# Performance work log

Hardware: AMD Instinct MI355X
Metric: run time of the kernel (lower is better)

The kernel has to match this reference:

```python
import jax, jax.numpy as jnp
import numpy as np

N_NODES = 100000


def _gcn_norm(edge_index, num_nodes):
    # Add self-loops, then symmetric normalization D^-1/2 A D^-1/2 (PyG gcn_norm).
    loops = jnp.arange(num_nodes, dtype=edge_index.dtype)
    src = jnp.concatenate([edge_index[0], loops])
    dst = jnp.concatenate([edge_index[1], loops])
    ew = jnp.ones(src.shape[0], dtype=jnp.float32)
    deg = jax.ops.segment_sum(ew, dst, num_segments=num_nodes)
    dinv = jnp.where(deg > 0, jax.lax.rsqrt(deg), 0.0)
    norm = dinv[src] * ew * dinv[dst]
    return src, dst, norm


def _prop_gcn_conv(x, W, b, src, dst, norm, num_nodes, prop_nums):
    # PropGCNConv: linear transform once, then prop_nums hops of normalized
    # sparse propagation (gather from src, scale, scatter-add to dst), + bias.
    x = x @ W
    for _ in range(prop_nums):
        msgs = x[src] * norm[:, None]              # [E, d]
        x = jax.ops.segment_sum(msgs, dst, num_segments=num_nodes)
    return x + b


def setup_inputs() -> dict:
    key = jax.random.key(0)
    k1, k2, k3, k4 = jax.random.split(key, 4)
    in_dim, hid_dim, num_classes = 128, 64, 40
    n_edges = 800000
    x = jax.random.normal(k1, (N_NODES, in_dim), dtype=jnp.float32)
    W0 = jax.random.normal(k2, (in_dim, hid_dim), dtype=jnp.float32) * (1.0 / np.sqrt(in_dim))
    b0 = jnp.zeros((hid_dim,), dtype=jnp.float32)
    Wc = jax.random.normal(k3, (hid_dim, num_classes), dtype=jnp.float32) * (1.0 / np.sqrt(hid_dim))
    bc = jnp.zeros((num_classes,), dtype=jnp.float32)
    edge_index = jax.random.randint(k4, (2, n_edges), 0, N_NODES, dtype=jnp.int64)
    return {"x": x, "W0": W0, "b0": b0, "Wc": Wc, "bc": bc,
            "edge_index": edge_index, "prop_nums": 30}


def reference(x, W0, b0, Wc, bc, edge_index, prop_nums):
    n = x.shape[0]
    src, dst, norm = _gcn_norm(edge_index, n)
    # feat_bottleneck: conv -> relu -> dropout (eval mode -> identity)
    h = _prop_gcn_conv(x, W0, b0, src, dst, norm, n, prop_nums)
    h = jax.nn.relu(h)
    # feat_classifier: single-hop PropGCNConv
    out = _prop_gcn_conv(h, Wc, bc, src, dst, norm, n, 1)
    return out
```

## Files before the change

### kernel.cpp

```cpp
#include <hip/hip_runtime.h>

#define NN  100000
#define NE  800000
#define NNZ 900000
#define IN_DIM 128
#define HID 64
#define NC  40
#define HOPS 30

typedef _Float16 half8 __attribute__((ext_vector_type(8)));


__global__ void init_cnt_k(int* __restrict__ cnt) {
    int i = blockIdx.x * blockDim.x + threadIdx.x;
    if (i < NN) cnt[i] = 1;
}

__global__ void count_edges_k(const int* __restrict__ dst, int* __restrict__ cnt) {
    int e = blockIdx.x * blockDim.x + threadIdx.x;
    if (e < NE) atomicAdd(&cnt[dst[e]], 1);
}

__global__ void dinv_k(const int* __restrict__ cnt, float* __restrict__ dinv) {
    int i = blockIdx.x * blockDim.x + threadIdx.x;
    if (i < NN) dinv[i] = rsqrtf((float)cnt[i]);
}

__global__ void scan_blocks_k(const int* __restrict__ cnt, int* __restrict__ rp,
                              int* __restrict__ partials) {
    __shared__ int s[256];
    int tid = threadIdx.x;
    int i = blockIdx.x * 256 + tid;
    int v = (i < NN) ? cnt[i] : 0;
    s[tid] = v;
    __syncthreads();
    for (int off = 1; off < 256; off <<= 1) {
        int t = (tid >= off) ? s[tid - off] : 0;
        __syncthreads();
        s[tid] += t;
        __syncthreads();
    }
    if (i < NN) rp[i] = s[tid] - v;
    if (tid == 255) partials[blockIdx.x] = s[255];
}

__global__ void scan_partials_k(int* __restrict__ partials, int nblk) {
    if (blockIdx.x == 0 && threadIdx.x == 0) {
        int acc = 0;
        for (int b = 0; b < nblk; ++b) { int t = partials[b]; partials[b] = acc; acc += t; }
    }
}

__global__ void add_offsets_k(int* __restrict__ rp, const int* __restrict__ partials) {
    int i = blockIdx.x * 256 + threadIdx.x;
    if (i < NN) rp[i] += partials[blockIdx.x];
    if (i == 0) rp[NN] = NNZ;
}

__global__ void fill_csr_k(const int* __restrict__ src, const int* __restrict__ dst,
                           const float* __restrict__ dinv, const int* __restrict__ rp,
                           int* __restrict__ cursor, int2* __restrict__ cv) {
    int e = blockIdx.x * blockDim.x + threadIdx.x;
    if (e >= NNZ) return;
    int s, d;
    if (e < NE) { s = src[e]; d = dst[e]; }
    else        { s = d = e - NE; }
    int pos = rp[d] + atomicAdd(&cursor[d], 1);
    int2 p;
    p.x = s;
    p.y = __float_as_int(dinv[s] * dinv[d]);
    cv[pos] = p;
}


__global__ void __launch_bounds__(256, 4) gemm1_k(const float* __restrict__ x,
                                                  const float* __restrict__ W,
                                                  _Float16* __restrict__ out) {
    __shared__ float Ws[IN_DIM * HID];
    int t = threadIdx.x;
    for (int i = t; i < IN_DIM * HID / 4; i += 256)
        ((float4*)Ws)[i] = ((const float4*)W)[i];
    __syncthreads();
    int node = blockIdx.x * 256 + t;
    if (node >= NN) return;
    const float4* xr = (const float4*)(x + (size_t)node * IN_DIM);
    float4 acc[16];
#pragma unroll
    for (int c = 0; c < 16; ++c) acc[c] = make_float4(0.f, 0.f, 0.f, 0.f);
#pragma unroll 4
    for (int k4 = 0; k4 < IN_DIM / 4; ++k4) {
        float4 xv = xr[k4];
#pragma unroll
        for (int kk = 0; kk < 4; ++kk) {
            float xs = (kk == 0) ? xv.x : (kk == 1) ? xv.y : (kk == 2) ? xv.z : xv.w;
            const float4* wr = (const float4*)(Ws + (k4 * 4 + kk) * HID);
#pragma unroll
            for (int c4 = 0; c4 < 16; ++c4) {
                float4 wv = wr[c4];
                acc[c4].x = fmaf(xs, wv.x, acc[c4].x);
                acc[c4].y = fmaf(xs, wv.y, acc[c4].y);
                acc[c4].z = fmaf(xs, wv.z, acc[c4].z);
                acc[c4].w = fmaf(xs, wv.w, acc[c4].w);
            }
        }
    }
    half8* o8 = (half8*)(out + (size_t)node * HID);
#pragma unroll
    for (int g = 0; g < 8; ++g) {
        half8 o;
        float4 lo = acc[g * 2], hi = acc[g * 2 + 1];
        o[0] = (_Float16)lo.x; o[1] = (_Float16)lo.y; o[2] = (_Float16)lo.z; o[3] = (_Float16)lo.w;
        o[4] = (_Float16)hi.x; o[5] = (_Float16)hi.y; o[6] = (_Float16)hi.z; o[7] = (_Float16)hi.w;
        o8[g] = o;
    }
}

__global__ void prop64_k(const _Float16* __restrict__ xin, _Float16* __restrict__ xout,
                         const int* __restrict__ rp, const int2* __restrict__ cv) {
    int wid  = threadIdx.x >> 6;
    int lane = threadIdx.x & 63;
    int n    = lane >> 5;
    int s    = (lane >> 3) & 3;
    int f    = lane & 7;
    int node = blockIdx.x * 8 + wid * 2 + n;
    int beg = rp[node], end = rp[node + 1];
    const half8* x8 = (const half8*)xin;
    float a0 = 0.f, a1 = 0.f, a2 = 0.f, a3 = 0.f, a4 = 0.f, a5 = 0.f, a6 = 0.f, a7 = 0.f;
    for (int e = beg + s; e < end; e += 16) {
        int  e1 = e + 4,  e2 = e + 8,  e3 = e + 12;
        bool p1 = e1 < end, p2 = e2 < end, p3 = e3 < end;
        int2 q0 = cv[e];
        int2 q1 = cv[p1 ? e1 : beg];
        int2 q2 = cv[p2 ? e2 : beg];
        int2 q3 = cv[p3 ? e3 : beg];
        float v0 = __int_as_float(q0.y);
        float v1 = p1 ? __int_as_float(q1.y) : 0.f;
        float v2 = p2 ? __int_as_float(q2.y) : 0.f;
        float v3 = p3 ? __int_as_float(q3.y) : 0.f;
        half8 x0 = x8[(size_t)q0.x * 8 + f];
        half8 x1 = x8[(size_t)q1.x * 8 + f];
        half8 x2 = x8[(size_t)q2.x * 8 + f];
        half8 x3 = x8[(size_t)q3.x * 8 + f];
        a0 += v0 * (float)x0[0] + v1 * (float)x1[0] + v2 * (float)x2[0] + v3 * (float)x3[0];
        a1 += v0 * (float)x0[1] + v1 * (float)x1[1] + v2 * (float)x2[1] + v3 * (float)x3[1];
        a2 += v0 * (float)x0[2] + v1 * (float)x1[2] + v2 * (float)x2[2] + v3 * (float)x3[2];
        a3 += v0 * (float)x0[3] + v1 * (float)x1[3] + v2 * (float)x2[3] + v3 * (float)x3[3];
        a4 += v0 * (float)x0[4] + v1 * (float)x1[4] + v2 * (float)x2[4] + v3 * (float)x3[4];
        a5 += v0 * (float)x0[5] + v1 * (float)x1[5] + v2 * (float)x2[5] + v3 * (float)x3[5];
        a6 += v0 * (float)x0[6] + v1 * (float)x1[6] + v2 * (float)x2[6] + v3 * (float)x3[6];
        a7 += v0 * (float)x0[7] + v1 * (float)x1[7] + v2 * (float)x2[7] + v3 * (float)x3[7];
    }
#pragma unroll
    for (int m = 8; m <= 16; m <<= 1) {
        a0 += __shfl_xor(a0, m); a1 += __shfl_xor(a1, m);
        a2 += __shfl_xor(a2, m); a3 += __shfl_xor(a3, m);
        a4 += __shfl_xor(a4, m); a5 += __shfl_xor(a5, m);
        a6 += __shfl_xor(a6, m); a7 += __shfl_xor(a7, m);
    }
    if (s == 0) {
        half8 r;
        r[0] = (_Float16)a0; r[1] = (_Float16)a1; r[2] = (_Float16)a2; r[3] = (_Float16)a3;
        r[4] = (_Float16)a4; r[5] = (_Float16)a5; r[6] = (_Float16)a6; r[7] = (_Float16)a7;
        ((half8*)xout)[(size_t)node * 8 + f] = r;
    }
}

__global__ void __launch_bounds__(256, 4) gemm2_k(const _Float16* __restrict__ h,
                                                  const float* __restrict__ b0,
                                                  const float* __restrict__ Wc,
                                                  float* __restrict__ g) {
    __shared__ float Wcs[HID * NC];
    __shared__ float b0s[HID];
    int t = threadIdx.x;
    for (int i = t; i < HID * NC / 4; i += 256)
        ((float4*)Wcs)[i] = ((const float4*)Wc)[i];
    if (t < HID) b0s[t] = b0[t];
    __syncthreads();
    int node = blockIdx.x * 256 + t;
    if (node >= NN) return;
    const half8* hr = (const half8*)(h + (size_t)node * HID);
    float acc[NC];
#pragma unroll
    for (int c = 0; c < NC; ++c) acc[c] = 0.f;
#pragma unroll
    for (int j = 0; j < 8; ++j) {
        half8 hv = hr[j];
#pragma unroll
        for (int m = 0; m < 8; ++m) {
            int k = j * 8 + m;
            float fv = fmaxf((float)hv[m] + b0s[k], 0.f);
            const float4* wr = (const float4*)(Wcs + k * NC);
#pragma unroll
            for (int c4 = 0; c4 < NC / 4; ++c4) {
                float4 wv = wr[c4];
                acc[c4 * 4 + 0] = fmaf(fv, wv.x, acc[c4 * 4 + 0]);
                acc[c4 * 4 + 1] = fmaf(fv, wv.y, acc[c4 * 4 + 1]);
                acc[c4 * 4 + 2] = fmaf(fv, wv.z, acc[c4 * 4 + 2]);
                acc[c4 * 4 + 3] = fmaf(fv, wv.w, acc[c4 * 4 + 3]);
            }
        }
    }
    float4* go = (float4*)(g + (size_t)node * NC);
#pragma unroll
    for (int c4 = 0; c4 < NC / 4; ++c4) {
        float4 o; o.x = acc[c4 * 4 + 0]; o.y = acc[c4 * 4 + 1];
        o.z = acc[c4 * 4 + 2]; o.w = acc[c4 * 4 + 3];
        go[c4] = o;
    }
}

__global__ void prop40_k(const float* __restrict__ g, float* __restrict__ out,
                         const int* __restrict__ rp, const int2* __restrict__ cv,
                         const float* __restrict__ bc) {
    int t = blockIdx.x * 256 + threadIdx.x;
    int node = t >> 6;
    int lane = threadIdx.x & 63;
    int s = lane >> 3;
    int f = lane & 7;
    int beg = rp[node], end = rp[node + 1];
    float a0 = 0.f, a1 = 0.f, a2 = 0.f, a3 = 0.f, a4 = 0.f;
    for (int e = beg + s; e < end; e += 16) {
        int  e1 = e + 8;
        bool p1 = e1 < end;
        int2 q0 = cv[e];
        int2 q1 = cv[p1 ? e1 : beg];
        float v0 = __int_as_float(q0.y);
        float v1 = p1 ? __int_as_float(q1.y) : 0.f;
        const float* g0 = g + (size_t)q0.x * NC + f;
        const float* g1 = g + (size_t)q1.x * NC + f;
        a0 += v0 * g0[0]  + v1 * g1[0];
        a1 += v0 * g0[8]  + v1 * g1[8];
        a2 += v0 * g0[16] + v1 * g1[16];
        a3 += v0 * g0[24] + v1 * g1[24];
        a4 += v0 * g0[32] + v1 * g1[32];
    }
    for (int m = 8; m <= 32; m <<= 1) {
        a0 += __shfl_xor(a0, m); a1 += __shfl_xor(a1, m); a2 += __shfl_xor(a2, m);
        a3 += __shfl_xor(a3, m); a4 += __shfl_xor(a4, m);
    }
    if (s == 0) {
        float* o = out + (size_t)node * NC + f;
        o[0]  = a0 + bc[f];
        o[8]  = a1 + bc[f + 8];
        o[16] = a2 + bc[f + 16];
        o[24] = a3 + bc[f + 24];
        o[32] = a4 + bc[f + 32];
    }
}


extern "C" void kernel_launch(void* const* d_in, const int* in_sizes, int n_in,
                              void* d_out, int out_size, void* d_ws, size_t ws_size,
                              hipStream_t stream) {
    const float* x  = (const float*)d_in[0];
    const float* W0 = (const float*)d_in[1];
    const float* b0 = (const float*)d_in[2];
    const float* Wc = (const float*)d_in[3];
    const float* bc = (const float*)d_in[4];
    const int*   ei = (const int*)d_in[5];
    const int* src = ei;
    const int* dst = ei + NE;

    char* ws = (char*)d_ws;
    size_t off = 0;
    auto alloc = [&](size_t bytes) -> void* {
        void* p = ws + off;
        off = (off + bytes + 255) & ~(size_t)255;
        return p;
    };
    float* dinv     = (float*)alloc((size_t)NN * 4);
    int*   rp       = (int*)  alloc((size_t)(NN + 1) * 4);
    int*   cnt      = (int*)  alloc((size_t)NN * 4);
    int*   cursor   = (int*)  alloc((size_t)NN * 4);
    int*   partials = (int*)  alloc(512 * 4);
    int2*  cvp      = (int2*) alloc((size_t)NNZ * 8);
    _Float16* XA    = (_Float16*)alloc((size_t)NN * HID * 2);
    _Float16* XB    = (_Float16*)alloc((size_t)NN * HID * 2);
    float* G        = (float*)alloc((size_t)NN * NC * 4);

    const int nblk_n = (NN + 255) / 256;

    init_cnt_k   <<<nblk_n, 256, 0, stream>>>(cnt);
    count_edges_k<<<(NE + 255) / 256, 256, 0, stream>>>(dst, cnt);
    dinv_k       <<<nblk_n, 256, 0, stream>>>(cnt, dinv);
    scan_blocks_k<<<nblk_n, 256, 0, stream>>>(cnt, rp, partials);
    scan_partials_k<<<1, 64, 0, stream>>>(partials, nblk_n);
    add_offsets_k<<<nblk_n, 256, 0, stream>>>(rp, partials);
    hipMemsetAsync(cursor, 0, (size_t)NN * 4, stream);
    fill_csr_k   <<<(NNZ + 255) / 256, 256, 0, stream>>>(src, dst, dinv, rp, cursor, cvp);

    gemm1_k<<<nblk_n, 256, 0, stream>>>(x, W0, XA);

    _Float16* a = XA;
    _Float16* b = XB;
    for (int hop = 0; hop < HOPS; ++hop) {
        prop64_k<<<NN / 8, 256, 0, stream>>>(a, b, rp, cvp);
        _Float16* tmp = a; a = b; b = tmp;
    }

    gemm2_k<<<nblk_n, 256, 0, stream>>>(a, b0, Wc, G);
    prop40_k<<<NN * HID / 256, 256, 0, stream>>>(G, (float*)d_out, rp, cvp, bc);
}
```

Measured before the change: 887.6 us.

## Reuse degree counters as CSR cursors, retile gemm1, store classifier logits in fp16

The CSR build now zeroes the degree counters with a memset and folds the self-loop into later reads. It then decrements those counters to place edges, which removes the separate cursor array and the init kernel. gemm1 is retiled so each thread computes half the output columns for two nodes, sharing shared-memory weight reads across them. The classifier intermediate G is stored as fp16 and gathered as half8 vectors in the final propagation, halving that gather traffic at some precision cost.

```diff
diff --git a/kernel.cpp b/kernel.cpp
--- a/kernel.cpp
+++ b/kernel.cpp
@@ -11,11 +11,6 @@
 typedef _Float16 half8 __attribute__((ext_vector_type(8)));
 
 
-__global__ void init_cnt_k(int* __restrict__ cnt) {
-    int i = blockIdx.x * blockDim.x + threadIdx.x;
-    if (i < NN) cnt[i] = 1;
-}
-
 __global__ void count_edges_k(const int* __restrict__ dst, int* __restrict__ cnt) {
     int e = blockIdx.x * blockDim.x + threadIdx.x;
     if (e < NE) atomicAdd(&cnt[dst[e]], 1);
@@ -23,7 +18,7 @@
 
 __global__ void dinv_k(const int* __restrict__ cnt, float* __restrict__ dinv) {
     int i = blockIdx.x * blockDim.x + threadIdx.x;
-    if (i < NN) dinv[i] = rsqrtf((float)cnt[i]);
+    if (i < NN) dinv[i] = rsqrtf((float)(cnt[i] + 1));
 }
 
 __global__ void scan_blocks_k(const int* __restrict__ cnt, int* __restrict__ rp,
@@ -31,7 +26,7 @@
     __shared__ int s[256];
     int tid = threadIdx.x;
     int i = blockIdx.x * 256 + tid;
-    int v = (i < NN) ? cnt[i] : 0;
+    int v = (i < NN) ? (cnt[i] + 1) : 0;
     s[tid] = v;
     __syncthreads();
     for (int off = 1; off < 256; off <<= 1) {
@@ -59,21 +54,28 @@
 
 __global__ void fill_csr_k(const int* __restrict__ src, const int* __restrict__ dst,
                            const float* __restrict__ dinv, const int* __restrict__ rp,
-                           int* __restrict__ cursor, int2* __restrict__ cv) {
+                           int* __restrict__ cnt, int2* __restrict__ cv) {
     int e = blockIdx.x * blockDim.x + threadIdx.x;
     if (e >= NNZ) return;
-    int s, d;
-    if (e < NE) { s = src[e]; d = dst[e]; }
-    else        { s = d = e - NE; }
-    int pos = rp[d] + atomicAdd(&cursor[d], 1);
+    int pos;
     int2 p;
-    p.x = s;
-    p.y = __float_as_int(dinv[s] * dinv[d]);
+    if (e < NE) {
+        int s = src[e], d = dst[e];
+        int old = atomicAdd(&cnt[d], -1);
+        pos = rp[d] + old - 1;
+        p.x = s;
+        p.y = __float_as_int(dinv[s] * dinv[d]);
+    } else {
+        int i = e - NE;
+        pos = rp[i + 1] - 1;
+        p.x = i;
+        p.y = __float_as_int(dinv[i] * dinv[i]);
+    }
     cv[pos] = p;
 }
 
 
-__global__ void __launch_bounds__(256, 4) gemm1_k(const float* __restrict__ x,
+__global__ void __launch_bounds__(256, 2) gemm1_k(const float* __restrict__ x,
                                                   const float* __restrict__ W,
                                                   _Float16* __restrict__ out) {
     __shared__ float Ws[IN_DIM * HID];
@@ -81,37 +83,64 @@
     for (int i = t; i < IN_DIM * HID / 4; i += 256)
         ((float4*)Ws)[i] = ((const float4*)W)[i];
     __syncthreads();
-    int node = blockIdx.x * 256 + t;
-    if (node >= NN) return;
-    const float4* xr = (const float4*)(x + (size_t)node * IN_DIM);
-    float4 acc[16];
-#pragma unroll
-    for (int c = 0; c < 16; ++c) acc[c] = make_float4(0.f, 0.f, 0.f, 0.f);
-#pragma unroll 4
+    int w = t >> 6, l = t & 63;
+    int ch = w >> 1;
+    int n0 = blockIdx.x * 256 + (w & 1) * 64 + l;
+    int n1 = n0 + 128;
+    int n0c = n0 < NN ? n0 : NN - 1;
+    int n1c = n1 < NN ? n1 : NN - 1;
+    const float4* xr0 = (const float4*)(x + (size_t)n0c * IN_DIM);
+    const float4* xr1 = (const float4*)(x + (size_t)n1c * IN_DIM);
+    float4 a0[8], a1[8];
+#pragma unroll
+    for (int c = 0; c < 8; ++c) {
+        a0[c] = make_float4(0.f, 0.f, 0.f, 0.f);
+        a1[c] = make_float4(0.f, 0.f, 0.f, 0.f);
+    }
+#pragma unroll 2
     for (int k4 = 0; k4 < IN_DIM / 4; ++k4) {
-        float4 xv = xr[k4];
+        float4 xv0 = xr0[k4];
+        float4 xv1 = xr1[k4];
 #pragma unroll
         for (int kk = 0; kk < 4; ++kk) {
-            float xs = (kk == 0) ? xv.x : (kk == 1) ? xv.y : (kk == 2) ? xv.z : xv.w;
-            const float4* wr = (const float4*)(Ws + (k4 * 4 + kk) * HID);
-#pragma unroll
-            for (int c4 = 0; c4 < 16; ++c4) {
-                float4 wv = wr[c4];
-                acc[c4].x = fmaf(xs, wv.x, acc[c4].x);
-                acc[c4].y = fmaf(xs, wv.y, acc[c4].y);
-                acc[c4].z = fmaf(xs, wv.z, acc[c4].z);
-                acc[c4].w = fmaf(xs, wv.w, acc[c4].w);
+            float xs0 = (kk == 0) ? xv0.x : (kk == 1) ? xv0.y : (kk == 2) ? xv0.z : xv0.w;
+            float xs1 = (kk == 0) ? xv1.x : (kk == 1) ? xv1.y : (kk == 2) ? xv1.z : xv1.w;
+            const float4* wr = (const float4*)(Ws + (k4 * 4 + kk) * HID + ch * 32);
+#pragma unroll
+            for (int c = 0; c < 8; ++c) {
+                float4 wv = wr[c];
+                a0[c].x = fmaf(xs0, wv.x, a0[c].x);
+                a0[c].y = fmaf(xs0, wv.y, a0[c].y);
+                a0[c].z = fmaf(xs0, wv.z, a0[c].z);
+                a0[c].w = fmaf(xs0, wv.w, a0[c].w);
+                a1[c].x = fmaf(xs1, wv.x, a1[c].x);
+                a1[c].y = fmaf(xs1, wv.y, a1[c].y);
+                a1[c].z = fmaf(xs1, wv.z, a1[c].z);
+                a1[c].w = fmaf(xs1, wv.w, a1[c].w);
             }
         }
     }
-    half8* o8 = (half8*)(out + (size_t)node * HID);
-#pragma unroll
-    for (int g = 0; g < 8; ++g) {
-        half8 o;
-        float4 lo = acc[g * 2], hi = acc[g * 2 + 1];
-        o[0] = (_Float16)lo.x; o[1] = (_Float16)lo.y; o[2] = (_Float16)lo.z; o[3] = (_Float16)lo.w;
-        o[4] = (_Float16)hi.x; o[5] = (_Float16)hi.y; o[6] = (_Float16)hi.z; o[7] = (_Float16)hi.w;
-        o8[g] = o;
+    if (n0 < NN) {
+        half8* o = (half8*)(out + (size_t)n0 * HID + ch * 32);
+#pragma unroll
+        for (int g = 0; g < 4; ++g) {
+            half8 r;
+            float4 lo = a0[g * 2], hi = a0[g * 2 + 1];
+            r[0] = (_Float16)lo.x; r[1] = (_Float16)lo.y; r[2] = (_Float16)lo.z; r[3] = (_Float16)lo.w;
+            r[4] = (_Float16)hi.x; r[5] = (_Float16)hi.y; r[6] = (_Float16)hi.z; r[7] = (_Float16)hi.w;
+            o[g] = r;
+        }
+    }
+    if (n1 < NN) {
+        half8* o = (half8*)(out + (size_t)n1 * HID + ch * 32);
+#pragma unroll
+        for (int g = 0; g < 4; ++g) {
+            half8 r;
+            float4 lo = a1[g * 2], hi = a1[g * 2 + 1];
+            r[0] = (_Float16)lo.x; r[1] = (_Float16)lo.y; r[2] = (_Float16)lo.z; r[3] = (_Float16)lo.w;
+            r[4] = (_Float16)hi.x; r[5] = (_Float16)hi.y; r[6] = (_Float16)hi.z; r[7] = (_Float16)hi.w;
+            o[g] = r;
+        }
     }
 }
 
@@ -168,7 +197,7 @@
 __global__ void __launch_bounds__(256, 4) gemm2_k(const _Float16* __restrict__ h,
                                                   const float* __restrict__ b0,
                                                   const float* __restrict__ Wc,
-                                                  float* __restrict__ g) {
+                                                  _Float16* __restrict__ g) {
     __shared__ float Wcs[HID * NC];
     __shared__ float b0s[HID];
     int t = threadIdx.x;
@@ -200,16 +229,17 @@
             }
         }
     }
-    float4* go = (float4*)(g + (size_t)node * NC);
-#pragma unroll
-    for (int c4 = 0; c4 < NC / 4; ++c4) {
-        float4 o; o.x = acc[c4 * 4 + 0]; o.y = acc[c4 * 4 + 1];
-        o.z = acc[c4 * 4 + 2]; o.w = acc[c4 * 4 + 3];
-        go[c4] = o;
-    }
-}
-
-__global__ void prop40_k(const float* __restrict__ g, float* __restrict__ out,
+    half8* go = (half8*)(g + (size_t)node * NC);
+#pragma unroll
+    for (int j = 0; j < 5; ++j) {
+        half8 r;
+#pragma unroll
+        for (int m = 0; m < 8; ++m) r[m] = (_Float16)acc[j * 8 + m];
+        go[j] = r;
+    }
+}
+
+__global__ void prop40_k(const _Float16* __restrict__ g, float* __restrict__ out,
                          const int* __restrict__ rp, const int2* __restrict__ cv,
                          const float* __restrict__ bc) {
     int t = blockIdx.x * 256 + threadIdx.x;
@@ -218,7 +248,9 @@
     int s = lane >> 3;
     int f = lane & 7;
     int beg = rp[node], end = rp[node + 1];
-    float a0 = 0.f, a1 = 0.f, a2 = 0.f, a3 = 0.f, a4 = 0.f;
+    const half8* g8 = (const half8*)g;
+    bool act = f < 5;
+    float a0 = 0.f, a1 = 0.f, a2 = 0.f, a3 = 0.f, a4 = 0.f, a5 = 0.f, a6 = 0.f, a7 = 0.f;
     for (int e = beg + s; e < end; e += 16) {
         int  e1 = e + 8;
         bool p1 = e1 < end;
@@ -226,25 +258,36 @@
         int2 q1 = cv[p1 ? e1 : beg];
         float v0 = __int_as_float(q0.y);
         float v1 = p1 ? __int_as_float(q1.y) : 0.f;
-        const float* g0 = g + (size_t)q0.x * NC + f;
-        const float* g1 = g + (size_t)q1.x * NC + f;
-        a0 += v0 * g0[0]  + v1 * g1[0];
-        a1 += v0 * g0[8]  + v1 * g1[8];
-        a2 += v0 * g0[16] + v1 * g1[16];
-        a3 += v0 * g0[24] + v1 * g1[24];
-        a4 += v0 * g0[32] + v1 * g1[32];
-    }
+        if (act) {
+            half8 x0 = g8[(size_t)q0.x * 5 + f];
+            half8 x1 = g8[(size_t)q1.x * 5 + f];
+            a0 += v0 * (float)x0[0] + v1 * (float)x1[0];
+            a1 += v0 * (float)x0[1] + v1 * (float)x1[1];
+            a2 += v0 * (float)x0[2] + v1 * (float)x1[2];
+            a3 += v0 * (float)x0[3] + v1 * (float)x1[3];
+            a4 += v0 * (float)x0[4] + v1 * (float)x1[4];
+            a5 += v0 * (float)x0[5] + v1 * (float)x1[5];
+            a6 += v0 * (float)x0[6] + v1 * (float)x1[6];
+            a7 += v0 * (float)x0[7] + v1 * (float)x1[7];
+        }
+    }
+#pragma unroll
     for (int m = 8; m <= 32; m <<= 1) {
-        a0 += __shfl_xor(a0, m); a1 += __shfl_xor(a1, m); a2 += __shfl_xor(a2, m);
-        a3 += __shfl_xor(a3, m); a4 += __shfl_xor(a4, m);
-    }
-    if (s == 0) {
-        float* o = out + (size_t)node * NC + f;
-        o[0]  = a0 + bc[f];
-        o[8]  = a1 + bc[f + 8];
-        o[16] = a2 + bc[f + 16];
-        o[24] = a3 + bc[f + 24];
-        o[32] = a4 + bc[f + 32];
+        a0 += __shfl_xor(a0, m); a1 += __shfl_xor(a1, m);
+        a2 += __shfl_xor(a2, m); a3 += __shfl_xor(a3, m);
+        a4 += __shfl_xor(a4, m); a5 += __shfl_xor(a5, m);
+        a6 += __shfl_xor(a6, m); a7 += __shfl_xor(a7, m);
+    }
+    if (s == 0 && act) {
+        float* o = out + (size_t)node * NC + f * 8;
+        o[0] = a0 + bc[f * 8 + 0];
+        o[1] = a1 + bc[f * 8 + 1];
+        o[2] = a2 + bc[f * 8 + 2];
+        o[3] = a3 + bc[f * 8 + 3];
+        o[4] = a4 + bc[f * 8 + 4];
+        o[5] = a5 + bc[f * 8 + 5];
+        o[6] = a6 + bc[f * 8 + 6];
+        o[7] = a7 + bc[f * 8 + 7];
     }
 }
 
@@ -271,23 +314,21 @@
     float* dinv     = (float*)alloc((size_t)NN * 4);
     int*   rp       = (int*)  alloc((size_t)(NN + 1) * 4);
     int*   cnt      = (int*)  alloc((size_t)NN * 4);
-    int*   cursor   = (int*)  alloc((size_t)NN * 4);
     int*   partials = (int*)  alloc(512 * 4);
     int2*  cvp      = (int2*) alloc((size_t)NNZ * 8);
     _Float16* XA    = (_Float16*)alloc((size_t)NN * HID * 2);
     _Float16* XB    = (_Float16*)alloc((size_t)NN * HID * 2);
-    float* G        = (float*)alloc((size_t)NN * NC * 4);
+    _Float16* G     = (_Float16*)alloc((size_t)NN * NC * 2);
 
     const int nblk_n = (NN + 255) / 256;
 
-    init_cnt_k   <<<nblk_n, 256, 0, stream>>>(cnt);
+    hipMemsetAsync(cnt, 0, (size_t)NN * 4, stream);
     count_edges_k<<<(NE + 255) / 256, 256, 0, stream>>>(dst, cnt);
     dinv_k       <<<nblk_n, 256, 0, stream>>>(cnt, dinv);
     scan_blocks_k<<<nblk_n, 256, 0, stream>>>(cnt, rp, partials);
     scan_partials_k<<<1, 64, 0, stream>>>(partials, nblk_n);
     add_offsets_k<<<nblk_n, 256, 0, stream>>>(rp, partials);
-    hipMemsetAsync(cursor, 0, (size_t)NN * 4, stream);
-    fill_csr_k   <<<(NNZ + 255) / 256, 256, 0, stream>>>(src, dst, dinv, rp, cursor, cvp);
+    fill_csr_k   <<<(NNZ + 255) / 256, 256, 0, stream>>>(src, dst, dinv, rp, cnt, cvp);
 
     gemm1_k<<<nblk_n, 256, 0, stream>>>(x, W0, XA);
 
```

Measured after the change: 880.2 us. Within noise of the previous version (-0.8%).
